# Kernel tuning notes

Measured on AMD Instinct MI355X. Metric: run time of the kernel, lower is better.

Reference implementation:

```python
import jax, jax.numpy as jnp
import numpy as np

N_ATOMS = 100000
N_EDGES = 800000
ATOM_DIM = 32
BOND_DIM = 16


def setup_inputs() -> dict:
    key = jax.random.key(0)
    k1, k2, k3, k4 = jax.random.split(key, 4)
    atom_features = jax.random.normal(k1, (N_ATOMS, ATOM_DIM), dtype=jnp.float32)
    bond_features = jax.random.normal(k2, (N_EDGES, BOND_DIM), dtype=jnp.float32)
    pair_indices = jax.random.randint(k3, (N_EDGES, 2), 0, N_ATOMS, dtype=jnp.int64 if jax.config.jax_enable_x64 else jnp.int32)
    # glorot-uniform-ish kernel
    limit = np.sqrt(6.0 / (BOND_DIM + ATOM_DIM * ATOM_DIM))
    kernel = jax.random.uniform(k4, (BOND_DIM, ATOM_DIM * ATOM_DIM), dtype=jnp.float32, minval=-limit, maxval=limit)
    bias = jnp.zeros((ATOM_DIM * ATOM_DIM,), dtype=jnp.float32)
    return {"atom_features": atom_features, "bond_features": bond_features,
            "pair_indices": pair_indices, "kernel": kernel, "bias": bias}


def reference(atom_features, bond_features, pair_indices, kernel, bias):
    atom_dim = atom_features.shape[-1]
    n_atoms = atom_features.shape[0]
    # bond-conditioned per-edge transform matrices: [E, atom_dim, atom_dim]
    bt = (bond_features @ kernel + bias).reshape(-1, atom_dim, atom_dim)
    # gather neighbor atom features: [E, atom_dim]
    neigh = atom_features[pair_indices[:, 1]]
    # per-edge small matmul: messages [E, atom_dim]
    messages = jnp.einsum('eij,ej->ei', bt, neigh)
    # scatter-add to destination atoms
    aggregated = jax.ops.segment_sum(messages, pair_indices[:, 0], num_segments=n_atoms)
    return aggregated
```

## Files before the change

kernel.cpp:

```cpp
#include <hip/hip_runtime.h>
#include <hip/hip_bf16.h>

typedef __attribute__((ext_vector_type(8))) short short8;
typedef __attribute__((ext_vector_type(4))) short s16x4;
typedef __attribute__((ext_vector_type(4))) float f32x4;

#define N_ATOMS 100000
#define N_EDGES 800000
#define N_TILES (N_EDGES/16)
#define N_CHUNKS ((N_ATOMS + 255) / 256)

#define MSG_BLOCKS 768
#define MSG_WAVES  (MSG_BLOCKS*4)

#define WS_MSG     0ULL
#define WS_OFFS    51200000ULL
#define WS_COUNTS  51600016ULL
#define WS_RANK    58400016ULL
#define WS_PART    61600016ULL
#define WS_NEED    61602064ULL

__device__ __forceinline__ short f2bf(float x) {
    __hip_bfloat16 h = __float2bfloat16(x);
    return __builtin_bit_cast(short, h);
}
__device__ __forceinline__ float bf2f(short b) {
    unsigned u = ((unsigned)(unsigned short)b) << 16;
    return __builtin_bit_cast(float, u);
}

__global__ __launch_bounds__(256) void rank_kernel(const int2* __restrict__ pair,
                                                   int* __restrict__ counts,
                                                   int* __restrict__ rank) {
    int e = blockIdx.x * 256 + threadIdx.x;
    if (e < N_EDGES) rank[e] = atomicAdd(&counts[pair[e].x], 1);
}

__global__ __launch_bounds__(256) void scan_part(const int* __restrict__ counts,
                                                 int* __restrict__ partials) {
    const int tid = threadIdx.x;
    const int i = blockIdx.x * 256 + tid;
    int v = (i < N_ATOMS) ? counts[i] : 0;
#pragma unroll
    for (int off = 1; off < 64; off <<= 1) v += __shfl_xor(v, off);
    __shared__ int ws4[4];
    const int lane = tid & 63, wv = tid >> 6;
    if (lane == 0) ws4[wv] = v;
    __syncthreads();
    if (tid == 0) partials[blockIdx.x] = ws4[0] + ws4[1] + ws4[2] + ws4[3];
}

__global__ __launch_bounds__(512) void scan_mid(int* __restrict__ partials) {
    const int tid = threadIdx.x;
    const int lane = tid & 63, wv = tid >> 6;
    int v = (tid < N_CHUNKS) ? partials[tid] : 0;
    int inc = v;
#pragma unroll
    for (int off = 1; off < 64; off <<= 1) {
        int u = __shfl_up(inc, off);
        if (lane >= off) inc += u;
    }
    __shared__ int ws8[8];
    if (lane == 63) ws8[wv] = inc;
    __syncthreads();
    int base = 0;
#pragma unroll
    for (int k = 0; k < 8; ++k) base += (k < wv) ? ws8[k] : 0;
    if (tid < N_CHUNKS) partials[tid] = base + inc - v;
}

__global__ __launch_bounds__(256) void scan_final(const int* __restrict__ counts,
                                                  const int* __restrict__ partials,
                                                  int* __restrict__ offsets) {
    const int tid = threadIdx.x;
    const int i = blockIdx.x * 256 + tid;
    const int lane = tid & 63, wv = tid >> 6;
    int c = (i < N_ATOMS) ? counts[i] : 0;
    int inc = c;
#pragma unroll
    for (int off = 1; off < 64; off <<= 1) {
        int u = __shfl_up(inc, off);
        if (lane >= off) inc += u;
    }
    __shared__ int ws4[4];
    if (lane == 63) ws4[wv] = inc;
    __syncthreads();
    int base = partials[blockIdx.x];
#pragma unroll
    for (int k = 0; k < 4; ++k) base += (k < wv) ? ws4[k] : 0;
    const int off = base + inc - c;
    if (i < N_ATOMS) offsets[i] = off;
    if (i == N_ATOMS - 1) offsets[N_ATOMS] = off + c;
}

__global__ __launch_bounds__(256, 3)
void edge_msg_kernel(const float* __restrict__ atom,
                     const float* __restrict__ bond,
                     const float* __restrict__ kern,
                     const float* __restrict__ bias,
                     const int2*  __restrict__ pair,
                     const int*   __restrict__ rank,
                     const int*   __restrict__ offsets,
                     short*       __restrict__ msg)
{
    __shared__ __align__(16) short klds[17*2*512];
    __shared__ __align__(16) float blds[4*320];

    const int tid = threadIdx.x;
    for (int x = tid; x < 17*2*512; x += 256) {
        const int t = x & 7;
        const int l = (x >> 3) & 63;
        const int m = (x >> 9) & 1;
        const int b = x >> 10;
        const int i = m*16 + (l & 15);
        const int j = ((l >> 4) << 3) + t;
        const float v = (b < 16) ? kern[b*1024 + i*32 + j] : bias[i*32 + j];
        klds[x] = f2bf(v);
    }
    __syncthreads();

    const int wave = tid >> 6;
    const int lane = tid & 63;
    const int er   = lane & 15;
    const int jg   = lane >> 4;
    const int pid  = blockIdx.x * 4 + wave;

    short8 afr[16];
#pragma unroll
    for (int b = 0; b < 16; ++b)
        afr[b] = *(const short8*)&klds[b*1024 + lane*8];

    const int ibase = jg*4;

    float* bw = &blds[wave*320 + (lane >> 2)*20 + (lane & 3)*4];
    const float* brd = &blds[wave*320 + er*20];

    const int last = N_TILES - 1;

    const int t1p = min(pid + MSG_WAVES, last);
    int2  p0 = pair[pid*16 + er];
    int   r0 = rank[pid*16 + er];
    f32x4 bv0 = *(const f32x4*)(bond + pid*256 + lane*4);
    int2  p1 = pair[t1p*16 + er];
    int   r1 = rank[t1p*16 + er];
    f32x4 bv1 = *(const f32x4*)(bond + t1p*256 + lane*4);
    *(f32x4*)bw = bv0;
    int   o0 = offsets[p0.x];
    f32x4 n0 = *(const f32x4*)(atom + p0.y*32 + jg*8);
    f32x4 n1 = *(const f32x4*)(atom + p0.y*32 + jg*8 + 4);

    for (int t = pid; t < N_TILES; t += MSG_WAVES) {
        int koff = 0;
        asm volatile("" : "+v"(koff));

        const int t2 = min(t + 2*MSG_WAVES, last);
        const int2  p2  = pair[t2*16 + er];
        const int   r2  = rank[t2*16 + er];
        const f32x4 bv2 = *(const f32x4*)(bond + t2*256 + lane*4);

        const int   o1  = offsets[p1.x];
        const f32x4 n0n = *(const f32x4*)(atom + p1.y*32 + jg*8);
        const f32x4 n1n = *(const f32x4*)(atom + p1.y*32 + jg*8 + 4);

        short8 bfrag;
        bfrag[0]=f2bf(n0[0]); bfrag[1]=f2bf(n0[1]);
        bfrag[2]=f2bf(n0[2]); bfrag[3]=f2bf(n0[3]);
        bfrag[4]=f2bf(n1[0]); bfrag[5]=f2bf(n1[1]);
        bfrag[6]=f2bf(n1[2]); bfrag[7]=f2bf(n1[3]);

        f32x4 macc0 = {0.f,0.f,0.f,0.f};
        f32x4 macc1 = {0.f,0.f,0.f,0.f};
        const f32x4 z = {0.f,0.f,0.f,0.f};

#pragma unroll
        for (int g = 0; g < 4; ++g) {
            const f32x4 q = *(const f32x4*)(brd + g*4);
#pragma unroll
            for (int c = 0; c < 4; ++c) {
                const int b = g*4 + c;
                const short8 a1 = *(const short8*)&klds[b*1024 + 512 + lane*8 + koff];
                const f32x4 d0 = __builtin_amdgcn_mfma_f32_16x16x32_bf16(afr[b], bfrag, z, 0, 0, 0);
                const f32x4 d1 = __builtin_amdgcn_mfma_f32_16x16x32_bf16(a1,     bfrag, z, 0, 0, 0);
                macc0[0] = fmaf(q[c], d0[0], macc0[0]);
                macc0[1] = fmaf(q[c], d0[1], macc0[1]);
                macc0[2] = fmaf(q[c], d0[2], macc0[2]);
                macc0[3] = fmaf(q[c], d0[3], macc0[3]);
                macc1[0] = fmaf(q[c], d1[0], macc1[0]);
                macc1[1] = fmaf(q[c], d1[1], macc1[1]);
                macc1[2] = fmaf(q[c], d1[2], macc1[2]);
                macc1[3] = fmaf(q[c], d1[3], macc1[3]);
            }
        }
        {
            const short8 ab0 = *(const short8*)&klds[16*1024 +       lane*8 + koff];
            const short8 ab1 = *(const short8*)&klds[16*1024 + 512 + lane*8 + koff];
            const f32x4 d0 = __builtin_amdgcn_mfma_f32_16x16x32_bf16(ab0, bfrag, z, 0, 0, 0);
            const f32x4 d1 = __builtin_amdgcn_mfma_f32_16x16x32_bf16(ab1, bfrag, z, 0, 0, 0);
            macc0[0] += d0[0]; macc0[1] += d0[1]; macc0[2] += d0[2]; macc0[3] += d0[3];
            macc1[0] += d1[0]; macc1[1] += d1[1]; macc1[2] += d1[2]; macc1[3] += d1[3];
        }

        *(f32x4*)bw = bv1;

        const int sl = o0 + r0;
        s16x4 mv0, mv1;
        mv0[0]=f2bf(macc0[0]); mv0[1]=f2bf(macc0[1]);
        mv0[2]=f2bf(macc0[2]); mv0[3]=f2bf(macc0[3]);
        mv1[0]=f2bf(macc1[0]); mv1[1]=f2bf(macc1[1]);
        mv1[2]=f2bf(macc1[2]); mv1[3]=f2bf(macc1[3]);
        *(s16x4*)&msg[sl*32 + ibase]      = mv0;
        *(s16x4*)&msg[sl*32 + 16 + ibase] = mv1;

        p0 = p1; p1 = p2; r0 = r1; r1 = r2; o0 = o1; bv1 = bv2;
        n0 = n0n; n1 = n1n;
    }
}

__global__ __launch_bounds__(256) void gather_kernel(const short* __restrict__ msg,
                                                     const int* __restrict__ offsets,
                                                     float* __restrict__ out) {
    const int tid = threadIdx.x;
    const int a = blockIdx.x * 32 + (tid >> 3);
    const int sub = (tid & 7) * 4;
    if (a >= N_ATOMS) return;
    const int b0 = offsets[a], b1 = offsets[a + 1];
    f32x4 acc0 = {0.f, 0.f, 0.f, 0.f};
    f32x4 acc1 = {0.f, 0.f, 0.f, 0.f};
    int k = b0;
    for (; k + 1 < b1; k += 2) {
        s16x4 mv0 = *(const s16x4*)&msg[k*32 + sub];
        s16x4 mv1 = *(const s16x4*)&msg[(k+1)*32 + sub];
        acc0[0] += bf2f(mv0[0]); acc0[1] += bf2f(mv0[1]);
        acc0[2] += bf2f(mv0[2]); acc0[3] += bf2f(mv0[3]);
        acc1[0] += bf2f(mv1[0]); acc1[1] += bf2f(mv1[1]);
        acc1[2] += bf2f(mv1[2]); acc1[3] += bf2f(mv1[3]);
    }
    if (k < b1) {
        s16x4 mv0 = *(const s16x4*)&msg[k*32 + sub];
        acc0[0] += bf2f(mv0[0]); acc0[1] += bf2f(mv0[1]);
        acc0[2] += bf2f(mv0[2]); acc0[3] += bf2f(mv0[3]);
    }
    acc0[0] += acc1[0]; acc0[1] += acc1[1]; acc0[2] += acc1[2]; acc0[3] += acc1[3];
    *(f32x4*)&out[a*32 + sub] = acc0;
}

__global__ __launch_bounds__(256) void zero_out(f32x4* __restrict__ out) {
    int i = blockIdx.x * 256 + threadIdx.x;
    f32x4 z = {0.f, 0.f, 0.f, 0.f};
    out[i] = z;
}

__global__ __launch_bounds__(256, 4)
void edge_kernel_atomic(const float* __restrict__ atom, const float* __restrict__ bond,
                        const int2* __restrict__ pair, const float* __restrict__ kern,
                        const float* __restrict__ bias, float* __restrict__ out)
{
    __shared__ __align__(16) short alds[17*2*512];
    const int tid = threadIdx.x;
    for (int x = tid; x < 17*2*512; x += 256) {
        const int t = x & 7;
        const int l = (x >> 3) & 63;
        const int m = (x >> 9) & 1;
        const int b = x >> 10;
        const int i = m*16 + (l & 15);
        const int j = ((l >> 4) << 3) + t;
        const float v = (b < 16) ? kern[b*1024 + i*32 + j] : bias[i*32 + j];
        alds[x] = f2bf(v);
    }
    __syncthreads();
    const int wave = tid >> 6, lane = tid & 63;
    const int er = lane & 15, jg = lane >> 4;
    const int wid = blockIdx.x * 4 + wave;
    const int m = wid & 1, pid = wid >> 1;
    short8 afr[17];
#pragma unroll
    for (int b = 0; b < 17; ++b)
        afr[b] = *(const short8*)&alds[(b*2 + m)*512 + lane*8];
    const int ibase = m*16 + jg*4;
    for (int tile = pid; tile < N_TILES; tile += 2048) {
        const int e = tile*16 + er;
        const int2 p = pair[e];
        const f32x4* arow = (const f32x4*)(atom + p.y * 32);
        const f32x4 n0 = arow[jg*2];
        const f32x4 n1 = arow[jg*2 + 1];
        short8 bfrag;
        bfrag[0] = f2bf(n0[0]); bfrag[1] = f2bf(n0[1]);
        bfrag[2] = f2bf(n0[2]); bfrag[3] = f2bf(n0[3]);
        bfrag[4] = f2bf(n1[0]); bfrag[5] = f2bf(n1[1]);
        bfrag[6] = f2bf(n1[2]); bfrag[7] = f2bf(n1[3]);
        const f32x4* brow = (const f32x4*)(bond + e * 16);
        const f32x4 q0 = brow[0], q1 = brow[1], q2 = brow[2], q3 = brow[3];
        float bb[17];
        bb[0]=q0[0];  bb[1]=q0[1];  bb[2]=q0[2];  bb[3]=q0[3];
        bb[4]=q1[0];  bb[5]=q1[1];  bb[6]=q1[2];  bb[7]=q1[3];
        bb[8]=q2[0];  bb[9]=q2[1];  bb[10]=q2[2]; bb[11]=q2[3];
        bb[12]=q3[0]; bb[13]=q3[1]; bb[14]=q3[2]; bb[15]=q3[3];
        bb[16]=1.0f;
        f32x4 macc = {0.f,0.f,0.f,0.f};
#pragma unroll
        for (int b = 0; b < 17; ++b) {
            f32x4 z = {0.f,0.f,0.f,0.f};
            f32x4 d = __builtin_amdgcn_mfma_f32_16x16x32_bf16(afr[b], bfrag, z, 0, 0, 0);
            macc[0] = fmaf(bb[b], d[0], macc[0]);
            macc[1] = fmaf(bb[b], d[1], macc[1]);
            macc[2] = fmaf(bb[b], d[2], macc[2]);
            macc[3] = fmaf(bb[b], d[3], macc[3]);
        }
        float* obase = out + p.x * 32 + ibase;
        atomicAdd(obase + 0, macc[0]);
        atomicAdd(obase + 1, macc[1]);
        atomicAdd(obase + 2, macc[2]);
        atomicAdd(obase + 3, macc[3]);
    }
}

extern "C" void kernel_launch(void* const* d_in, const int* in_sizes, int n_in,
                              void* d_out, int out_size, void* d_ws, size_t ws_size,
                              hipStream_t stream)
{
    (void)in_sizes; (void)n_in; (void)out_size;
    const float* atom = (const float*)d_in[0];
    const float* bond = (const float*)d_in[1];
    const int2*  pair = (const int2*)d_in[2];
    const float* kern = (const float*)d_in[3];
    const float* bias = (const float*)d_in[4];
    float* out = (float*)d_out;

    if (ws_size < WS_NEED) {
        zero_out<<<dim3(N_ATOMS*32/4/256), dim3(256), 0, stream>>>((f32x4*)out);
        edge_kernel_atomic<<<dim3(1024), dim3(256), 0, stream>>>(atom, bond, pair, kern, bias, out);
        return;
    }

    char* ws = (char*)d_ws;
    short* msg    = (short*)(ws + WS_MSG);
    int* offsets  = (int*)(ws + WS_OFFS);
    int* counts   = (int*)(ws + WS_COUNTS);
    int* rank     = (int*)(ws + WS_RANK);
    int* partials = (int*)(ws + WS_PART);

    const int eb = (N_EDGES + 255) / 256;
    hipMemsetAsync(counts, 0, N_ATOMS * sizeof(int), stream);
    rank_kernel<<<dim3(eb), dim3(256), 0, stream>>>(pair, counts, rank);
    scan_part<<<dim3(N_CHUNKS), dim3(256), 0, stream>>>(counts, partials);
    scan_mid<<<dim3(1), dim3(512), 0, stream>>>(partials);
    scan_final<<<dim3(N_CHUNKS), dim3(256), 0, stream>>>(counts, partials, offsets);
    edge_msg_kernel<<<dim3(MSG_BLOCKS), dim3(256), 0, stream>>>(atom, bond, kern, bias, pair, rank, offsets, msg);
    gather_kernel<<<dim3((N_ATOMS + 31)/32), dim3(256), 0, stream>>>(msg, offsets, out);
}
```

Before: 109.5 us.

## Switch edge message kernel to 32x32x16 MFMA tiles of 32 edges

After: 114.2 us. 4.3% more time.

```diff
diff --git a/kernel.cpp b/kernel.cpp
--- a/kernel.cpp
+++ b/kernel.cpp
@@ -4,10 +4,12 @@
 typedef __attribute__((ext_vector_type(8))) short short8;
 typedef __attribute__((ext_vector_type(4))) short s16x4;
 typedef __attribute__((ext_vector_type(4))) float f32x4;
+typedef __attribute__((ext_vector_type(16))) float f32x16;
 
 #define N_ATOMS 100000
 #define N_EDGES 800000
 #define N_TILES (N_EDGES/16)
+#define N_TILES32 (N_EDGES/32)
 #define N_CHUNKS ((N_ATOMS + 255) / 256)
 
 #define MSG_BLOCKS 768
@@ -104,16 +106,16 @@
                      short*       __restrict__ msg)
 {
     __shared__ __align__(16) short klds[17*2*512];
-    __shared__ __align__(16) float blds[4*320];
+    __shared__ __align__(16) float blds[4*32*20];
 
     const int tid = threadIdx.x;
     for (int x = tid; x < 17*2*512; x += 256) {
         const int t = x & 7;
         const int l = (x >> 3) & 63;
-        const int m = (x >> 9) & 1;
+        const int h = (x >> 9) & 1;
         const int b = x >> 10;
-        const int i = m*16 + (l & 15);
-        const int j = ((l >> 4) << 3) + t;
+        const int i = l & 31;
+        const int j = h*16 + ((l >> 5) << 3) + t;
         const float v = (b < 16) ? kern[b*1024 + i*32 + j] : bias[i*32 + j];
         klds[x] = f2bf(v);
     }
@@ -121,98 +123,103 @@
 
     const int wave = tid >> 6;
     const int lane = tid & 63;
-    const int er   = lane & 15;
-    const int jg   = lane >> 4;
+    const int el   = lane & 31;
+    const int hi   = lane >> 5;
     const int pid  = blockIdx.x * 4 + wave;
 
-    short8 afr[16];
-#pragma unroll
-    for (int b = 0; b < 16; ++b)
-        afr[b] = *(const short8*)&klds[b*1024 + lane*8];
-
-    const int ibase = jg*4;
-
-    float* bw = &blds[wave*320 + (lane >> 2)*20 + (lane & 3)*4];
-    const float* brd = &blds[wave*320 + er*20];
-
-    const int last = N_TILES - 1;
+    short8 afr[17];
+#pragma unroll
+    for (int b = 0; b < 17; ++b)
+        afr[b] = *(const short8*)&klds[(b*2 + 0)*512 + lane*8];
+
+    float* bw = &blds[wave*640 + (lane >> 1)*20 + (lane & 1)*8];
+    const float* brd = &blds[wave*640 + el*20];
+
+    const int last = N_TILES32 - 1;
 
     const int t1p = min(pid + MSG_WAVES, last);
-    int2  p0 = pair[pid*16 + er];
-    int   r0 = rank[pid*16 + er];
-    f32x4 bv0 = *(const f32x4*)(bond + pid*256 + lane*4);
-    int2  p1 = pair[t1p*16 + er];
-    int   r1 = rank[t1p*16 + er];
-    f32x4 bv1 = *(const f32x4*)(bond + t1p*256 + lane*4);
-    *(f32x4*)bw = bv0;
-    int   o0 = offsets[p0.x];
-    f32x4 n0 = *(const f32x4*)(atom + p0.y*32 + jg*8);
-    f32x4 n1 = *(const f32x4*)(atom + p0.y*32 + jg*8 + 4);
-
-    for (int t = pid; t < N_TILES; t += MSG_WAVES) {
+    int2 p0 = pair[pid*32 + el];
+    int  r0 = rank[pid*32 + el];
+    int2 p1 = pair[t1p*32 + el];
+    int  r1 = rank[t1p*32 + el];
+    {
+        const float* bsrc = bond + ((long long)pid*32 + (lane >> 1))*16 + (lane & 1)*8;
+        const f32x4 bva = *(const f32x4*)bsrc;
+        const f32x4 bvb = *(const f32x4*)(bsrc + 4);
+        *(f32x4*)bw = bva;
+        *(f32x4*)(bw + 4) = bvb;
+    }
+    int o0 = offsets[p0.x];
+    short8 b0f, b1f;
+    {
+        const float* ap = atom + p0.y*32 + hi*8;
+        const f32x4 na0 = *(const f32x4*)ap;
+        const f32x4 na1 = *(const f32x4*)(ap + 4);
+        const f32x4 nb0 = *(const f32x4*)(ap + 16);
+        const f32x4 nb1 = *(const f32x4*)(ap + 20);
+        b0f[0]=f2bf(na0[0]); b0f[1]=f2bf(na0[1]); b0f[2]=f2bf(na0[2]); b0f[3]=f2bf(na0[3]);
+        b0f[4]=f2bf(na1[0]); b0f[5]=f2bf(na1[1]); b0f[6]=f2bf(na1[2]); b0f[7]=f2bf(na1[3]);
+        b1f[0]=f2bf(nb0[0]); b1f[1]=f2bf(nb0[1]); b1f[2]=f2bf(nb0[2]); b1f[3]=f2bf(nb0[3]);
+        b1f[4]=f2bf(nb1[0]); b1f[5]=f2bf(nb1[1]); b1f[6]=f2bf(nb1[2]); b1f[7]=f2bf(nb1[3]);
+    }
+
+    for (int t = pid; t < N_TILES32; t += MSG_WAVES) {
         int koff = 0;
         asm volatile("" : "+v"(koff));
 
         const int t2 = min(t + 2*MSG_WAVES, last);
-        const int2  p2  = pair[t2*16 + er];
-        const int   r2  = rank[t2*16 + er];
-        const f32x4 bv2 = *(const f32x4*)(bond + t2*256 + lane*4);
-
+        const int2 p2 = pair[t2*32 + el];
+        const int  r2 = rank[t2*32 + el];
+
+        const int t1 = min(t + MSG_WAVES, last);
+        const float* bsrc = bond + ((long long)t1*32 + (lane >> 1))*16 + (lane & 1)*8;
+        const f32x4 bva = *(const f32x4*)bsrc;
+        const f32x4 bvb = *(const f32x4*)(bsrc + 4);
         const int   o1  = offsets[p1.x];
-        const f32x4 n0n = *(const f32x4*)(atom + p1.y*32 + jg*8);
-        const f32x4 n1n = *(const f32x4*)(atom + p1.y*32 + jg*8 + 4);
-
-        short8 bfrag;
-        bfrag[0]=f2bf(n0[0]); bfrag[1]=f2bf(n0[1]);
-        bfrag[2]=f2bf(n0[2]); bfrag[3]=f2bf(n0[3]);
-        bfrag[4]=f2bf(n1[0]); bfrag[5]=f2bf(n1[1]);
-        bfrag[6]=f2bf(n1[2]); bfrag[7]=f2bf(n1[3]);
-
-        f32x4 macc0 = {0.f,0.f,0.f,0.f};
-        f32x4 macc1 = {0.f,0.f,0.f,0.f};
-        const f32x4 z = {0.f,0.f,0.f,0.f};
-
+        const float* ap = atom + p1.y*32 + hi*8;
+        const f32x4 na0 = *(const f32x4*)ap;
+        const f32x4 na1 = *(const f32x4*)(ap + 4);
+        const f32x4 nb0 = *(const f32x4*)(ap + 16);
+        const f32x4 nb1 = *(const f32x4*)(ap + 20);
+
+        const f32x16 zz = {0.f,0.f,0.f,0.f,0.f,0.f,0.f,0.f,
+                           0.f,0.f,0.f,0.f,0.f,0.f,0.f,0.f};
+        const short8 ab1f = *(const short8*)&klds[(16*2 + 1)*512 + lane*8 + koff];
+        f32x16 macc = __builtin_amdgcn_mfma_f32_32x32x16_bf16(afr[16], b0f, zz, 0, 0, 0);
+        macc = __builtin_amdgcn_mfma_f32_32x32x16_bf16(ab1f, b1f, macc, 0, 0, 0);
 #pragma unroll
         for (int g = 0; g < 4; ++g) {
             const f32x4 q = *(const f32x4*)(brd + g*4);
 #pragma unroll
             for (int c = 0; c < 4; ++c) {
                 const int b = g*4 + c;
-                const short8 a1 = *(const short8*)&klds[b*1024 + 512 + lane*8 + koff];
-                const f32x4 d0 = __builtin_amdgcn_mfma_f32_16x16x32_bf16(afr[b], bfrag, z, 0, 0, 0);
-                const f32x4 d1 = __builtin_amdgcn_mfma_f32_16x16x32_bf16(a1,     bfrag, z, 0, 0, 0);
-                macc0[0] = fmaf(q[c], d0[0], macc0[0]);
-                macc0[1] = fmaf(q[c], d0[1], macc0[1]);
-                macc0[2] = fmaf(q[c], d0[2], macc0[2]);
-                macc0[3] = fmaf(q[c], d0[3], macc0[3]);
-                macc1[0] = fmaf(q[c], d1[0], macc1[0]);
-                macc1[1] = fmaf(q[c], d1[1], macc1[1]);
-                macc1[2] = fmaf(q[c], d1[2], macc1[2]);
-                macc1[3] = fmaf(q[c], d1[3], macc1[3]);
+                const short8 a1 = *(const short8*)&klds[(b*2 + 1)*512 + lane*8 + koff];
+                f32x16 d = __builtin_amdgcn_mfma_f32_32x32x16_bf16(afr[b], b0f, zz, 0, 0, 0);
+                d = __builtin_amdgcn_mfma_f32_32x32x16_bf16(a1, b1f, d, 0, 0, 0);
+#pragma unroll
+                for (int r = 0; r < 16; ++r)
+                    macc[r] = fmaf(q[c], d[r], macc[r]);
             }
         }
-        {
-            const short8 ab0 = *(const short8*)&klds[16*1024 +       lane*8 + koff];
-            const short8 ab1 = *(const short8*)&klds[16*1024 + 512 + lane*8 + koff];
-            const f32x4 d0 = __builtin_amdgcn_mfma_f32_16x16x32_bf16(ab0, bfrag, z, 0, 0, 0);
-            const f32x4 d1 = __builtin_amdgcn_mfma_f32_16x16x32_bf16(ab1, bfrag, z, 0, 0, 0);
-            macc0[0] += d0[0]; macc0[1] += d0[1]; macc0[2] += d0[2]; macc0[3] += d0[3];
-            macc1[0] += d1[0]; macc1[1] += d1[1]; macc1[2] += d1[2]; macc1[3] += d1[3];
+
+        *(f32x4*)bw = bva;
+        *(f32x4*)(bw + 4) = bvb;
+
+        b0f[0]=f2bf(na0[0]); b0f[1]=f2bf(na0[1]); b0f[2]=f2bf(na0[2]); b0f[3]=f2bf(na0[3]);
+        b0f[4]=f2bf(na1[0]); b0f[5]=f2bf(na1[1]); b0f[6]=f2bf(na1[2]); b0f[7]=f2bf(na1[3]);
+        b1f[0]=f2bf(nb0[0]); b1f[1]=f2bf(nb0[1]); b1f[2]=f2bf(nb0[2]); b1f[3]=f2bf(nb0[3]);
+        b1f[4]=f2bf(nb1[0]); b1f[5]=f2bf(nb1[1]); b1f[6]=f2bf(nb1[2]); b1f[7]=f2bf(nb1[3]);
+
+        const int sl = o0 + r0;
+#pragma unroll
+        for (int g = 0; g < 4; ++g) {
+            s16x4 mv;
+            mv[0]=f2bf(macc[4*g+0]); mv[1]=f2bf(macc[4*g+1]);
+            mv[2]=f2bf(macc[4*g+2]); mv[3]=f2bf(macc[4*g+3]);
+            *(s16x4*)&msg[sl*32 + g*8 + hi*4] = mv;
         }
 
-        *(f32x4*)bw = bv1;
-
-        const int sl = o0 + r0;
-        s16x4 mv0, mv1;
-        mv0[0]=f2bf(macc0[0]); mv0[1]=f2bf(macc0[1]);
-        mv0[2]=f2bf(macc0[2]); mv0[3]=f2bf(macc0[3]);
-        mv1[0]=f2bf(macc1[0]); mv1[1]=f2bf(macc1[1]);
-        mv1[2]=f2bf(macc1[2]); mv1[3]=f2bf(macc1[3]);
-        *(s16x4*)&msg[sl*32 + ibase]      = mv0;
-        *(s16x4*)&msg[sl*32 + 16 + ibase] = mv1;
-
-        p0 = p1; p1 = p2; r0 = r1; r1 = r2; o0 = o1; bv1 = bv2;
-        n0 = n0n; n1 = n1n;
+        p0 = p1; r0 = r1; o0 = o1; p1 = p2; r1 = r2;
     }
 }
 
```

## Replace three-pass prefix scan with single-pass decoupled lookback scan

Applied to the files above, without the earlier changes.

New measurement: 123.2 us. 1.13x slower.

```diff
diff --git a/kernel.cpp b/kernel.cpp
--- a/kernel.cpp
+++ b/kernel.cpp
@@ -36,59 +36,52 @@
     if (e < N_EDGES) rank[e] = atomicAdd(&counts[pair[e].x], 1);
 }
 
-__global__ __launch_bounds__(256) void scan_part(const int* __restrict__ counts,
-                                                 int* __restrict__ partials) {
+__global__ __launch_bounds__(256) void scan_lookback(const int* __restrict__ counts,
+                                                     int* __restrict__ offsets,
+                                                     int* __restrict__ state) {
+    const int b   = blockIdx.x;
     const int tid = threadIdx.x;
-    const int i = blockIdx.x * 256 + tid;
-    int v = (i < N_ATOMS) ? counts[i] : 0;
-#pragma unroll
-    for (int off = 1; off < 64; off <<= 1) v += __shfl_xor(v, off);
-    __shared__ int ws4[4];
+    const int i   = b * 256 + tid;
     const int lane = tid & 63, wv = tid >> 6;
-    if (lane == 0) ws4[wv] = v;
-    __syncthreads();
-    if (tid == 0) partials[blockIdx.x] = ws4[0] + ws4[1] + ws4[2] + ws4[3];
-}
-
-__global__ __launch_bounds__(512) void scan_mid(int* __restrict__ partials) {
-    const int tid = threadIdx.x;
-    const int lane = tid & 63, wv = tid >> 6;
-    int v = (tid < N_CHUNKS) ? partials[tid] : 0;
-    int inc = v;
+
+    int c = (i < N_ATOMS) ? counts[i] : 0;
+    int inc = c;
 #pragma unroll
     for (int off = 1; off < 64; off <<= 1) {
         int u = __shfl_up(inc, off);
         if (lane >= off) inc += u;
     }
-    __shared__ int ws8[8];
-    if (lane == 63) ws8[wv] = inc;
-    __syncthreads();
-    int base = 0;
-#pragma unroll
-    for (int k = 0; k < 8; ++k) base += (k < wv) ? ws8[k] : 0;
-    if (tid < N_CHUNKS) partials[tid] = base + inc - v;
-}
-
-__global__ __launch_bounds__(256) void scan_final(const int* __restrict__ counts,
-                                                  const int* __restrict__ partials,
-                                                  int* __restrict__ offsets) {
-    const int tid = threadIdx.x;
-    const int i = blockIdx.x * 256 + tid;
-    const int lane = tid & 63, wv = tid >> 6;
-    int c = (i < N_ATOMS) ? counts[i] : 0;
-    int inc = c;
-#pragma unroll
-    for (int off = 1; off < 64; off <<= 1) {
-        int u = __shfl_up(inc, off);
-        if (lane >= off) inc += u;
-    }
     __shared__ int ws4[4];
+    __shared__ int sprefix;
     if (lane == 63) ws4[wv] = inc;
     __syncthreads();
-    int base = partials[blockIdx.x];
-#pragma unroll
-    for (int k = 0; k < 4; ++k) base += (k < wv) ? ws4[k] : 0;
-    const int off = base + inc - c;
+    int wbase = 0;
+#pragma unroll
+    for (int k = 0; k < 4; ++k) wbase += (k < wv) ? ws4[k] : 0;
+
+    if (tid == 0) {
+        const int agg = ws4[0] + ws4[1] + ws4[2] + ws4[3];
+        if (b == 0) {
+            atomicExch(&state[0], (agg << 2) | 2);
+            sprefix = 0;
+        } else {
+            atomicExch(&state[b], (agg << 2) | 1);
+            int run = 0, j = b - 1;
+            while (true) {
+                const int s = atomicAdd(&state[j], 0);
+                const int f = s & 3;
+                if (f == 0) continue;
+                run += (s >> 2);
+                if (f == 2) break;
+                --j;
+            }
+            atomicExch(&state[b], ((run + agg) << 2) | 2);
+            sprefix = run;
+        }
+    }
+    __syncthreads();
+
+    const int off = sprefix + wbase + inc - c;
     if (i < N_ATOMS) offsets[i] = off;
     if (i == N_ATOMS - 1) offsets[N_ATOMS] = off + c;
 }
@@ -337,14 +330,13 @@
     int* offsets  = (int*)(ws + WS_OFFS);
     int* counts   = (int*)(ws + WS_COUNTS);
     int* rank     = (int*)(ws + WS_RANK);
-    int* partials = (int*)(ws + WS_PART);
+    int* state    = (int*)(ws + WS_PART);
 
     const int eb = (N_EDGES + 255) / 256;
     hipMemsetAsync(counts, 0, N_ATOMS * sizeof(int), stream);
+    hipMemsetAsync(state, 0, N_CHUNKS * sizeof(int), stream);
     rank_kernel<<<dim3(eb), dim3(256), 0, stream>>>(pair, counts, rank);
-    scan_part<<<dim3(N_CHUNKS), dim3(256), 0, stream>>>(counts, partials);
-    scan_mid<<<dim3(1), dim3(512), 0, stream>>>(partials);
-    scan_final<<<dim3(N_CHUNKS), dim3(256), 0, stream>>>(counts, partials, offsets);
+    scan_lookback<<<dim3(N_CHUNKS), dim3(256), 0, stream>>>(counts, offsets, state);
     edge_msg_kernel<<<dim3(MSG_BLOCKS), dim3(256), 0, stream>>>(atom, bond, kern, bias, pair, rank, offsets, msg);
     gather_kernel<<<dim3((N_ATOMS + 31)/32), dim3(256), 0, stream>>>(msg, offsets, out);
 }
```
